# Performance work log

Hardware: AMD Instinct MI355X
Metric: run time of the kernel (lower is better)

The kernel has to match this reference:

```python
import jax, jax.numpy as jnp
import numpy as np
from jax.scipy.special import logsumexp

B, T, H, S = 32, 2000, 256, 63  # batch, time steps, hidden dim, num_states (=num_classes)


def setup_inputs() -> dict:
    key = jax.random.key(0)
    ks = jax.random.split(key, 5)
    return {
        "ctc_logits": jax.random.normal(ks[0], (B, T, S), dtype=jnp.float32),
        "frame_embeddings": jax.random.normal(ks[1], (B, T, H), dtype=jnp.float32),
        "keyword_tokens": jax.random.randint(ks[2], (B, 32), 0, S),
        "W1": jax.random.normal(ks[3], (2 * H, H), dtype=jnp.float32) * 0.02,
        "b1": jnp.zeros((H,), dtype=jnp.float32),
        "W2": jax.random.normal(ks[4], (H, S), dtype=jnp.float32) * 0.02,
        "b2": jnp.zeros((S,), dtype=jnp.float32),
    }


def reference(ctc_logits, frame_embeddings, keyword_tokens, W1, b1, W2, b2):
    Bv, Tv, Sv = ctc_logits.shape
    logp = jax.nn.log_softmax(ctc_logits, axis=-1)  # (B,T,S)

    # transition scores for frame pair (t, t-1) <-> trans_all[t-1], batched over all t at once
    pairs = jnp.concatenate([frame_embeddings[:, 1:], frame_embeddings[:, :-1]], axis=-1)  # (B,T-1,2H)
    h = jax.nn.relu(jnp.einsum("bti,ij->btj", pairs, W1) + b1)
    trans = jnp.einsum("bti,ij->btj", h, W2) + b2  # (B,T-1,S)

    lp_t = jnp.swapaxes(logp, 0, 1)   # (T,B,S)
    tr_t = jnp.swapaxes(trans, 0, 1)  # (T-1,B,S)

    # forward recursion
    f0 = jnp.zeros((Bv, Sv), dtype=logp.dtype).at[:, 0].set(
        logp[jnp.arange(Bv), 0, keyword_tokens[:, 0]])

    def fstep(f_prev, x):
        lp, tr = x  # each (B,S)
        # [b,j,s] = f_prev[b,j] + lp[b,s] + tr[b,s]; reduce over j (prev state)
        scores = f_prev[:, :, None] + lp[:, None, :] + tr[:, None, :]
        f = logsumexp(scores, axis=1)
        return f, f

    _, f_rest = jax.lax.scan(fstep, f0, (lp_t[1:], tr_t))
    fwd = jnp.concatenate([f0[None], f_rest], axis=0)  # (T,B,S)

    # backward recursion (reverse scan); backward at t uses pair (t+1, t) = trans[t]
    bT = jnp.zeros((Bv, Sv), dtype=logp.dtype)

    def bstep(b_next, x):
        lp, tr = x  # lp = logp[t+1], tr = trans[t]
        # [b,s,k] = b_next[b,k] + lp[b,s] + tr[b,s]; reduce over k (next state)
        scores = b_next[:, None, :] + lp[:, :, None] + tr[:, :, None]
        b = logsumexp(scores, axis=2)
        return b, b

    _, b_rest = jax.lax.scan(bstep, bT, (lp_t[1:], tr_t), reverse=True)
    bwd = jnp.concatenate([b_rest, bT[None]], axis=0)  # (T,B,S)

    alignments = jax.nn.softmax(jnp.swapaxes(fwd + bwd, 0, 1), axis=-1)  # (B,T,S)
    return alignments
```

## Files before the change

kernel.cpp:

```cpp
#include <hip/hip_runtime.h>
#include <stdint.h>

#define NB 32
#define NT 2000
#define NH 256
#define NS 63
#define LDSROW 264

typedef __attribute__((ext_vector_type(8))) short bf16x8;
typedef __attribute__((ext_vector_type(4))) float f32x4;

__device__ inline unsigned short f2bf(float f) {
  union { float f; uint32_t u; } v; v.f = f;
  return (unsigned short)((v.u + 0x7fffu + ((v.u >> 16) & 1u)) >> 16);
}
__device__ inline unsigned int pk2(float a, float b) {
  return (unsigned int)f2bf(a) | ((unsigned int)f2bf(b) << 16);
}
__device__ inline bf16x8 pack8(const float* g) {
  union { bf16x8 v; unsigned int u[4]; } c;
  c.u[0] = pk2(g[0], g[1]); c.u[1] = pk2(g[2], g[3]);
  c.u[2] = pk2(g[4], g[5]); c.u[3] = pk2(g[6], g[7]);
  return c.v;
}

__device__ inline unsigned int pk2_hw(float a, float b) {
  unsigned int r;
  asm("v_cvt_pk_bf16_f32 %0, %1, %2" : "=v"(r) : "v"(a), "v"(b));
  return r;
}
__device__ inline unsigned short cvt1_hw(float a) {
  unsigned int r;
  asm("v_cvt_pk_bf16_f32 %0, %1, %1" : "=v"(r) : "v"(a));
  return (unsigned short)r;
}

#define NSLOT1 (16 * 4 * 4 * 64)
#define NSLOT2 (8 * 4 * 64)
#define WS_NEEDED ((size_t)(NSLOT1 + NSLOT2) * 16)

__global__ __launch_bounds__(256) void prep_weights(
    const float* __restrict__ W1, const float* __restrict__ W2,
    unsigned short* __restrict__ w1f, unsigned short* __restrict__ w2f) {
  const int tid = blockIdx.x * 256 + threadIdx.x;
  if (tid < NSLOT1) {
    const int lane = tid & 63;
    const int quad = lane >> 4, l16 = lane & 15;
    int r = tid >> 6;
    const int tn = r & 3; r >>= 2;
    const int wv = r & 3; r >>= 2;
    const int km = r;
    const int kb = (km >> 3) * 256 + (km & 7) * 32 + quad * 8;
    const int n = wv * 64 + tn * 16 + l16;
    ushort4 lo, hi;
    lo.x = f2bf(W1[(size_t)(kb + 0) * NH + n]);
    lo.y = f2bf(W1[(size_t)(kb + 1) * NH + n]);
    lo.z = f2bf(W1[(size_t)(kb + 2) * NH + n]);
    lo.w = f2bf(W1[(size_t)(kb + 3) * NH + n]);
    hi.x = f2bf(W1[(size_t)(kb + 4) * NH + n]);
    hi.y = f2bf(W1[(size_t)(kb + 5) * NH + n]);
    hi.z = f2bf(W1[(size_t)(kb + 6) * NH + n]);
    hi.w = f2bf(W1[(size_t)(kb + 7) * NH + n]);
    *(ushort4*)&w1f[(size_t)tid * 8] = lo;
    *(ushort4*)&w1f[(size_t)tid * 8 + 4] = hi;
  } else if (tid < NSLOT1 + NSLOT2) {
    const int t2 = tid - NSLOT1;
    const int lane = t2 & 63;
    const int quad = lane >> 4, l16 = lane & 15;
    const int tn = (t2 >> 6) & 3;
    const int ks = t2 >> 8;
    const int kb = ks * 32 + quad * 8;
    const int n = tn * 16 + l16;
    ushort4 lo = {0, 0, 0, 0}, hi = {0, 0, 0, 0};
    if (n < NS) {
      lo.x = f2bf(W2[(size_t)(kb + 0) * NS + n]);
      lo.y = f2bf(W2[(size_t)(kb + 1) * NS + n]);
      lo.z = f2bf(W2[(size_t)(kb + 2) * NS + n]);
      lo.w = f2bf(W2[(size_t)(kb + 3) * NS + n]);
      hi.x = f2bf(W2[(size_t)(kb + 4) * NS + n]);
      hi.y = f2bf(W2[(size_t)(kb + 5) * NS + n]);
      hi.z = f2bf(W2[(size_t)(kb + 6) * NS + n]);
      hi.w = f2bf(W2[(size_t)(kb + 7) * NS + n]);
    }
    *(ushort4*)&w2f[(size_t)t2 * 8] = lo;
    *(ushort4*)&w2f[(size_t)t2 * 8 + 4] = hi;
  }
}

template <bool PACKED>
__global__ __launch_bounds__(256, 4) void fused_kernel(
    const float* __restrict__ E, const float* __restrict__ logits,
    const int* __restrict__ kw,
    const float* __restrict__ W1, const float* __restrict__ W2,
    const unsigned short* __restrict__ w1f, const unsigned short* __restrict__ w2f,
    const float* __restrict__ b1, const float* __restrict__ b2,
    float* __restrict__ out) {
  const int b = blockIdx.y;
  const int a0 = blockIdx.x * 63;
  const int base = a0 - 1;
  const int tid = threadIdx.x;
  const int w = tid >> 6;
  const int lane = tid & 63;
  const int quad = lane >> 4;
  const int l16 = lane & 15;
  const int n0 = w * 64;

  __shared__ unsigned short lds[65 * LDSROW];

  const float* Eb = E + (size_t)b * NT * NH;
  const float* lb = logits + (size_t)b * NT * NS;

  #pragma unroll
  for (int it = 0; it < 16; ++it) {
    const int row = it * 4 + w;
    int tr = base + row;
    tr = (tr < 0) ? 0 : (tr > NT - 1 ? NT - 1 : tr);
    float4 v = *(const float4*)&Eb[(size_t)tr * NH + (lane << 2)];
    uint2 o;
    o.x = pk2_hw(v.x, v.y); o.y = pk2_hw(v.z, v.w);
    *(uint2*)&lds[row * LDSROW + (lane << 2)] = o;
  }
  if (tid < 64) {
    int tr = base + 64; if (tr > NT - 1) tr = NT - 1;
    float4 v = *(const float4*)&Eb[(size_t)tr * NH + (lane << 2)];
    uint2 o;
    o.x = pk2_hw(v.x, v.y); o.y = pk2_hw(v.z, v.w);
    *(uint2*)&lds[64 * LDSROW + (lane << 2)] = o;
  }
  __syncthreads();

  f32x4 acc[4][4];
  #pragma unroll
  for (int tm = 0; tm < 4; ++tm)
    #pragma unroll
    for (int tn = 0; tn < 4; ++tn) acc[tm][tn] = (f32x4){0.f, 0.f, 0.f, 0.f};

  if constexpr (PACKED) {
    const unsigned short* wbase = w1f + (size_t)(((w << 2) * 64) + lane) * 8;
#define W1F_AT(KM, TN) \
  (*(const bf16x8*)(wbase + ((size_t)((((KM) << 4) + (TN))) << 9)))
    bf16x8 cb0 = W1F_AT(0, 0), cb1 = W1F_AT(0, 1);
    bf16x8 cb2 = W1F_AT(0, 2), cb3 = W1F_AT(0, 3);
    __builtin_amdgcn_s_setprio(1);
    #pragma unroll
    for (int km = 0; km < 16; ++km) {
      bf16x8 nb0, nb1, nb2, nb3;
      if (km < 15) {
        nb0 = W1F_AT(km + 1, 0); nb1 = W1F_AT(km + 1, 1);
        nb2 = W1F_AT(km + 1, 2); nb3 = W1F_AT(km + 1, 3);
      }
      const int aoff = (km >> 3) ? 0 : 1;
      bf16x8 af[4];
      #pragma unroll
      for (int tm = 0; tm < 4; ++tm)
        af[tm] = *(const bf16x8*)&lds[(tm * 16 + l16 + aoff) * LDSROW +
                                      (km & 7) * 32 + quad * 8];
      #pragma unroll
      for (int tm = 0; tm < 4; ++tm)
        acc[tm][0] = __builtin_amdgcn_mfma_f32_16x16x32_bf16(af[tm], cb0, acc[tm][0], 0, 0, 0);
      #pragma unroll
      for (int tm = 0; tm < 4; ++tm)
        acc[tm][1] = __builtin_amdgcn_mfma_f32_16x16x32_bf16(af[tm], cb1, acc[tm][1], 0, 0, 0);
      #pragma unroll
      for (int tm = 0; tm < 4; ++tm)
        acc[tm][2] = __builtin_amdgcn_mfma_f32_16x16x32_bf16(af[tm], cb2, acc[tm][2], 0, 0, 0);
      #pragma unroll
      for (int tm = 0; tm < 4; ++tm)
        acc[tm][3] = __builtin_amdgcn_mfma_f32_16x16x32_bf16(af[tm], cb3, acc[tm][3], 0, 0, 0);
      if (km < 15) { cb0 = nb0; cb1 = nb1; cb2 = nb2; cb3 = nb3; }
    }
    __builtin_amdgcn_s_setprio(0);
#undef W1F_AT
  } else {
    const float* w1p = W1 + (size_t)(quad * 8) * NH + n0 + l16;
    #pragma unroll
    for (int km = 0; km < 16; ++km) {
      const int hk = (km >> 3) * 256 + (km & 7) * 32;
      const int aoff = (km >> 3) ? 0 : 1;
      bf16x8 af[4];
      #pragma unroll
      for (int tm = 0; tm < 4; ++tm)
        af[tm] = *(const bf16x8*)&lds[(tm * 16 + l16 + aoff) * LDSROW +
                                      (km & 7) * 32 + quad * 8];
      float g[8], gn[8];
      #pragma unroll
      for (int j = 0; j < 8; ++j) g[j] = w1p[(size_t)(hk + j) * NH];
      #pragma unroll
      for (int tn = 0; tn < 4; ++tn) {
        if (tn < 3) {
          #pragma unroll
          for (int j = 0; j < 8; ++j)
            gn[j] = w1p[(size_t)(hk + j) * NH + (tn + 1) * 16];
        }
        bf16x8 bq = pack8(g);
        #pragma unroll
        for (int tm = 0; tm < 4; ++tm)
          acc[tm][tn] = __builtin_amdgcn_mfma_f32_16x16x32_bf16(
              af[tm], bq, acc[tm][tn], 0, 0, 0);
        if (tn < 3) {
          #pragma unroll
          for (int j = 0; j < 8; ++j) g[j] = gn[j];
        }
      }
    }
  }
  __syncthreads();

  #pragma unroll
  for (int tn = 0; tn < 4; ++tn) {
    float b1v = b1[n0 + tn * 16 + l16];
    #pragma unroll
    for (int tm = 0; tm < 4; ++tm)
      #pragma unroll
      for (int r = 0; r < 4; ++r) {
        float hv = fmaxf(acc[tm][tn][r] + b1v, 0.f);
        lds[(tm * 16 + quad * 4 + r) * LDSROW + n0 + tn * 16 + l16] = cvt1_hw(hv);
      }
  }
  __syncthreads();

  const int m0 = w * 16;
  float lpv[16];
  #pragma unroll
  for (int tn = 0; tn < 4; ++tn) {
    const int s = tn * 16 + l16;
    const int cc = (s < NS) ? s : NS - 1;
    #pragma unroll
    for (int r = 0; r < 4; ++r) {
      int tt = a0 + m0 + quad * 4 + r;
      if (tt > NT - 1) tt = NT - 1;
      lpv[tn * 4 + r] = lb[(size_t)tt * NS + cc];
    }
  }

  f32x4 acc2[4];
  #pragma unroll
  for (int tn = 0; tn < 4; ++tn) acc2[tn] = (f32x4){0.f, 0.f, 0.f, 0.f};

  if constexpr (PACKED) {
    const unsigned short* w2base = w2f + (size_t)lane * 8;
    __builtin_amdgcn_s_setprio(1);
    #pragma unroll
    for (int ks = 0; ks < 8; ++ks) {
      bf16x8 af = *(const bf16x8*)&lds[(m0 + l16) * LDSROW + ks * 32 + quad * 8];
      #pragma unroll
      for (int tn = 0; tn < 4; ++tn) {
        bf16x8 bq = *(const bf16x8*)(w2base + ((size_t)((ks << 2) + tn) << 9));
        acc2[tn] = __builtin_amdgcn_mfma_f32_16x16x32_bf16(af, bq, acc2[tn], 0, 0, 0);
      }
    }
    __builtin_amdgcn_s_setprio(0);
  } else {
    #pragma unroll
    for (int ks = 0; ks < 8; ++ks) {
      const int k0 = ks * 32;
      bf16x8 af = *(const bf16x8*)&lds[(m0 + l16) * LDSROW + k0 + quad * 8];
      #pragma unroll
      for (int tn = 0; tn < 4; ++tn) {
        const int n = tn * 16 + l16;
        float g[8];
        #pragma unroll
        for (int j = 0; j < 8; ++j)
          g[j] = (n < NS) ? W2[(size_t)(k0 + quad * 8 + j) * NS + n] : 0.f;
        bf16x8 bq = pack8(g);
        acc2[tn] = __builtin_amdgcn_mfma_f32_16x16x32_bf16(af, bq, acc2[tn], 0, 0, 0);
      }
    }
  }

  {
    float* Uw = (float*)(lds + (size_t)m0 * LDSROW);
    #pragma unroll
    for (int tn = 0; tn < 4; ++tn) {
      const int s = tn * 16 + l16;
      const float b2v = (s < NS) ? b2[s] : 0.f;
      #pragma unroll
      for (int r = 0; r < 4; ++r)
        Uw[(quad * 4 + r) * 68 + s] = acc2[tn][r] + b2v + lpv[tn * 4 + r];
    }
  }
  __syncthreads();

  const float* Ur = (const float*)lds;
  if (a0 == 0 && w == 0) {
    float v = (lane < NS) ? lb[lane] : -1e30f;
    float m = v;
    #pragma unroll
    for (int o = 32; o > 0; o >>= 1) m = fmaxf(m, __shfl_xor(m, o));
    float ee = (lane < NS) ? __expf(v - m) : 0.f;
    float ss = ee;
    #pragma unroll
    for (int o = 32; o > 0; o >>= 1) ss += __shfl_xor(ss, o);
    const float lse = m + __logf(ss);
    const float f00 = lb[kw[b * 32]] - lse;
    float sc = ((lane == 0) ? f00 : 0.f) + Ur[68 + lane];
    float e = (lane < NS) ? __expf(sc) : 0.f;
    float s = e;
    #pragma unroll
    for (int o = 32; o > 0; o >>= 1) s += __shfl_xor(s, o);
    if (lane < NS)
      out[(size_t)b * NT * NS + lane] = e * __builtin_amdgcn_rcpf(s);
  }

  float ev[16], sm[16];
  #pragma unroll
  for (int rr = 0; rr < 16; ++rr) {
    const int j = m0 + rr;
    const int t = a0 + j;
    const bool valid = (j < 63) && (t < NT) && (t != 0);
    float u0 = valid ? Ur[(j >> 4) * 2112 + (j & 15) * 68 + lane] : 0.f;
    float u1 = (valid && t != NT - 1)
                   ? Ur[((j + 1) >> 4) * 2112 + ((j + 1) & 15) * 68 + lane]
                   : 0.f;
    ev[rr] = (valid && lane < NS) ? __expf(u0 + u1) : 0.f;
    sm[rr] = ev[rr];
  }
  #pragma unroll
  for (int o = 32; o > 0; o >>= 1) {
    #pragma unroll
    for (int rr = 0; rr < 16; ++rr) sm[rr] += __shfl_xor(sm[rr], o);
  }
  #pragma unroll
  for (int rr = 0; rr < 16; ++rr) {
    const int j = m0 + rr;
    const int t = a0 + j;
    const bool valid = (j < 63) && (t < NT) && (t != 0);
    if (valid && lane < NS)
      out[((size_t)b * NT + t) * NS + lane] = ev[rr] * __builtin_amdgcn_rcpf(sm[rr]);
  }
}

extern "C" void kernel_launch(void* const* d_in, const int* in_sizes, int n_in,
                              void* d_out, int out_size, void* d_ws, size_t ws_size,
                              hipStream_t stream) {
  const float* logits = (const float*)d_in[0];
  const float* E      = (const float*)d_in[1];
  const int*   kw     = (const int*)d_in[2];
  const float* W1     = (const float*)d_in[3];
  const float* b1     = (const float*)d_in[4];
  const float* W2     = (const float*)d_in[5];
  const float* b2     = (const float*)d_in[6];
  float* out = (float*)d_out;

  dim3 g(32, NB);

  if (ws_size >= WS_NEEDED && d_ws != nullptr) {
    unsigned short* w1f = (unsigned short*)d_ws;
    unsigned short* w2f = w1f + (size_t)NSLOT1 * 8;
    prep_weights<<<dim3((NSLOT1 + NSLOT2) / 256), 256, 0, stream>>>(W1, W2, w1f, w2f);
    fused_kernel<true><<<g, 256, 0, stream>>>(E, logits, kw, W1, W2, w1f, w2f,
                                              b1, b2, out);
  } else {
    fused_kernel<false><<<g, 256, 0, stream>>>(E, logits, kw, W1, W2, nullptr,
                                               nullptr, b1, b2, out);
  }
}
```

Baseline: 133.1 us.

## Overlap loading second half of embeddings with first-half MFMA compute

The packed path now stages only the first 128 feature columns of the frame-embedding tile into LDS before starting the matmul. It then runs the K-steps that use those columns while streaming the remaining 128 columns row-group by row-group into LDS, and finishes with the other K-steps after a barrier. The goal is to hide global-load latency of the embedding tile behind MFMA work. The cost is an extra barrier, a non-unrolled first loop without W1 prefetch, and more complex scheduling.

```diff
diff --git a/kernel.cpp b/kernel.cpp
--- a/kernel.cpp
+++ b/kernel.cpp
@@ -110,25 +110,6 @@
   const float* Eb = E + (size_t)b * NT * NH;
   const float* lb = logits + (size_t)b * NT * NS;
 
-  #pragma unroll
-  for (int it = 0; it < 16; ++it) {
-    const int row = it * 4 + w;
-    int tr = base + row;
-    tr = (tr < 0) ? 0 : (tr > NT - 1 ? NT - 1 : tr);
-    float4 v = *(const float4*)&Eb[(size_t)tr * NH + (lane << 2)];
-    uint2 o;
-    o.x = pk2_hw(v.x, v.y); o.y = pk2_hw(v.z, v.w);
-    *(uint2*)&lds[row * LDSROW + (lane << 2)] = o;
-  }
-  if (tid < 64) {
-    int tr = base + 64; if (tr > NT - 1) tr = NT - 1;
-    float4 v = *(const float4*)&Eb[(size_t)tr * NH + (lane << 2)];
-    uint2 o;
-    o.x = pk2_hw(v.x, v.y); o.y = pk2_hw(v.z, v.w);
-    *(uint2*)&lds[64 * LDSROW + (lane << 2)] = o;
-  }
-  __syncthreads();
-
   f32x4 acc[4][4];
   #pragma unroll
   for (int tm = 0; tm < 4; ++tm)
@@ -136,25 +117,48 @@
     for (int tn = 0; tn < 4; ++tn) acc[tm][tn] = (f32x4){0.f, 0.f, 0.f, 0.f};
 
   if constexpr (PACKED) {
+    const int r2 = lane >> 5;
+    const int cf = (lane & 31) << 2;
+    #pragma unroll
+    for (int it = 0; it < 8; ++it) {
+      const int row = it * 8 + (w << 1) + r2;
+      int tr = base + row;
+      tr = (tr < 0) ? 0 : (tr > NT - 1 ? NT - 1 : tr);
+      float4 v = *(const float4*)&Eb[(size_t)tr * NH + cf];
+      uint2 o; o.x = pk2_hw(v.x, v.y); o.y = pk2_hw(v.z, v.w);
+      *(uint2*)&lds[row * LDSROW + cf] = o;
+    }
+    if (tid < 32) {
+      int tr = base + 64; if (tr > NT - 1) tr = NT - 1;
+      float4 v = *(const float4*)&Eb[(size_t)tr * NH + cf];
+      uint2 o; o.x = pk2_hw(v.x, v.y); o.y = pk2_hw(v.z, v.w);
+      *(uint2*)&lds[64 * LDSROW + cf] = o;
+    }
+    __syncthreads();
+
     const unsigned short* wbase = w1f + (size_t)(((w << 2) * 64) + lane) * 8;
 #define W1F_AT(KM, TN) \
   (*(const bf16x8*)(wbase + ((size_t)((((KM) << 4) + (TN))) << 9)))
-    bf16x8 cb0 = W1F_AT(0, 0), cb1 = W1F_AT(0, 1);
-    bf16x8 cb2 = W1F_AT(0, 2), cb3 = W1F_AT(0, 3);
-    __builtin_amdgcn_s_setprio(1);
-    #pragma unroll
-    for (int km = 0; km < 16; ++km) {
-      bf16x8 nb0, nb1, nb2, nb3;
-      if (km < 15) {
-        nb0 = W1F_AT(km + 1, 0); nb1 = W1F_AT(km + 1, 1);
-        nb2 = W1F_AT(km + 1, 2); nb3 = W1F_AT(km + 1, 3);
-      }
+
+    float4 sv;
+    {
+      const int row0 = (w << 1) + r2;
+      int tr = base + row0;
+      tr = (tr < 0) ? 0 : (tr > NT - 1 ? NT - 1 : tr);
+      sv = *(const float4*)&Eb[(size_t)tr * NH + 128 + cf];
+    }
+    #pragma unroll 1
+    for (int kk = 0; kk < 8; ++kk) {
+      const int km = kk + ((kk >> 2) << 2);
       const int aoff = (km >> 3) ? 0 : 1;
+      bf16x8 cb0 = W1F_AT(km, 0), cb1 = W1F_AT(km, 1);
+      bf16x8 cb2 = W1F_AT(km, 2), cb3 = W1F_AT(km, 3);
       bf16x8 af[4];
       #pragma unroll
       for (int tm = 0; tm < 4; ++tm)
         af[tm] = *(const bf16x8*)&lds[(tm * 16 + l16 + aoff) * LDSROW +
                                       (km & 7) * 32 + quad * 8];
+      __builtin_amdgcn_s_setprio(1);
       #pragma unroll
       for (int tm = 0; tm < 4; ++tm)
         acc[tm][0] = __builtin_amdgcn_mfma_f32_16x16x32_bf16(af[tm], cb0, acc[tm][0], 0, 0, 0);
@@ -167,11 +171,83 @@
       #pragma unroll
       for (int tm = 0; tm < 4; ++tm)
         acc[tm][3] = __builtin_amdgcn_mfma_f32_16x16x32_bf16(af[tm], cb3, acc[tm][3], 0, 0, 0);
-      if (km < 15) { cb0 = nb0; cb1 = nb1; cb2 = nb2; cb3 = nb3; }
-    }
-    __builtin_amdgcn_s_setprio(0);
+      __builtin_amdgcn_s_setprio(0);
+      {
+        const int row = kk * 8 + (w << 1) + r2;
+        uint2 o; o.x = pk2_hw(sv.x, sv.y); o.y = pk2_hw(sv.z, sv.w);
+        *(uint2*)&lds[row * LDSROW + 128 + cf] = o;
+        if (kk < 7) {
+          const int nrow = (kk + 1) * 8 + (w << 1) + r2;
+          int tr = base + nrow;
+          tr = (tr < 0) ? 0 : (tr > NT - 1 ? NT - 1 : tr);
+          sv = *(const float4*)&Eb[(size_t)tr * NH + 128 + cf];
+        }
+      }
+    }
+    if (tid < 32) {
+      int tr = base + 64; if (tr > NT - 1) tr = NT - 1;
+      float4 v = *(const float4*)&Eb[(size_t)tr * NH + 128 + cf];
+      uint2 o; o.x = pk2_hw(v.x, v.y); o.y = pk2_hw(v.z, v.w);
+      *(uint2*)&lds[64 * LDSROW + 128 + cf] = o;
+    }
+    __syncthreads();
+
+    {
+      bf16x8 cb0 = W1F_AT(4, 0), cb1 = W1F_AT(4, 1);
+      bf16x8 cb2 = W1F_AT(4, 2), cb3 = W1F_AT(4, 3);
+      __builtin_amdgcn_s_setprio(1);
+      #pragma unroll
+      for (int kk = 0; kk < 8; ++kk) {
+        const int km = kk + 4 + ((kk >> 2) << 2);
+        bf16x8 nb0, nb1, nb2, nb3;
+        if (kk < 7) {
+          const int kn = (kk + 1) + 4 + (((kk + 1) >> 2) << 2);
+          nb0 = W1F_AT(kn, 0); nb1 = W1F_AT(kn, 1);
+          nb2 = W1F_AT(kn, 2); nb3 = W1F_AT(kn, 3);
+        }
+        const int aoff = (km >> 3) ? 0 : 1;
+        bf16x8 af[4];
+        #pragma unroll
+        for (int tm = 0; tm < 4; ++tm)
+          af[tm] = *(const bf16x8*)&lds[(tm * 16 + l16 + aoff) * LDSROW +
+                                        (km & 7) * 32 + quad * 8];
+        #pragma unroll
+        for (int tm = 0; tm < 4; ++tm)
+          acc[tm][0] = __builtin_amdgcn_mfma_f32_16x16x32_bf16(af[tm], cb0, acc[tm][0], 0, 0, 0);
+        #pragma unroll
+        for (int tm = 0; tm < 4; ++tm)
+          acc[tm][1] = __builtin_amdgcn_mfma_f32_16x16x32_bf16(af[tm], cb1, acc[tm][1], 0, 0, 0);
+        #pragma unroll
+        for (int tm = 0; tm < 4; ++tm)
+          acc[tm][2] = __builtin_amdgcn_mfma_f32_16x16x32_bf16(af[tm], cb2, acc[tm][2], 0, 0, 0);
+        #pragma unroll
+        for (int tm = 0; tm < 4; ++tm)
+          acc[tm][3] = __builtin_amdgcn_mfma_f32_16x16x32_bf16(af[tm], cb3, acc[tm][3], 0, 0, 0);
+        if (kk < 7) { cb0 = nb0; cb1 = nb1; cb2 = nb2; cb3 = nb3; }
+      }
+      __builtin_amdgcn_s_setprio(0);
+    }
 #undef W1F_AT
   } else {
+    #pragma unroll
+    for (int it = 0; it < 16; ++it) {
+      const int row = it * 4 + w;
+      int tr = base + row;
+      tr = (tr < 0) ? 0 : (tr > NT - 1 ? NT - 1 : tr);
+      float4 v = *(const float4*)&Eb[(size_t)tr * NH + (lane << 2)];
+      uint2 o;
+      o.x = pk2_hw(v.x, v.y); o.y = pk2_hw(v.z, v.w);
+      *(uint2*)&lds[row * LDSROW + (lane << 2)] = o;
+    }
+    if (tid < 64) {
+      int tr = base + 64; if (tr > NT - 1) tr = NT - 1;
+      float4 v = *(const float4*)&Eb[(size_t)tr * NH + (lane << 2)];
+      uint2 o;
+      o.x = pk2_hw(v.x, v.y); o.y = pk2_hw(v.z, v.w);
+      *(uint2*)&lds[64 * LDSROW + (lane << 2)] = o;
+    }
+    __syncthreads();
+
     const float* w1p = W1 + (size_t)(quad * 8) * NH + n0 + l16;
     #pragma unroll
     for (int km = 0; km < 16; ++km) {
```

New measurement: 133.5 us. Within noise of the previous version (+0.3%).
